# Kernel optimization log

Hardware: AMD Instinct MI355X
Metric: run time of the kernel (lower is better)

## Reference

```python
import jax, jax.numpy as jnp
import numpy as np

TEMPERATURE = 0.07
EPS = 1e-8
LAMBDA_CONTRASTIVE = 0.3
AMBIGUOUS_THRESHOLD = 0.05
LABEL_SMOOTHING = 0.1

B, D, NUM_DIMS, NUM_PIECES = 4096, 256, 19, 1024


def setup_inputs() -> dict:
    key = jax.random.key(0)
    ks = jax.random.split(key, 7)
    return {
        "z_a": jax.random.normal(ks[0], (B, D), dtype=jnp.float32),
        "z_b": jax.random.normal(ks[1], (B, D), dtype=jnp.float32),
        "ranking_logits": jax.random.normal(ks[2], (B, NUM_DIMS), dtype=jnp.float32),
        "labels_a": jax.random.uniform(ks[3], (B, NUM_DIMS), dtype=jnp.float32),
        "labels_b": jax.random.uniform(ks[4], (B, NUM_DIMS), dtype=jnp.float32),
        "piece_ids_a": jax.random.randint(ks[5], (B,), 0, NUM_PIECES, dtype=jnp.int64 if jax.config.jax_enable_x64 else jnp.int32),
        "piece_ids_b": jax.random.randint(ks[6], (B,), 0, NUM_PIECES, dtype=jnp.int64 if jax.config.jax_enable_x64 else jnp.int32),
    }


def _infonce(embeddings, piece_ids, temperature=TEMPERATURE, eps=EPS):
    # embeddings [N, D], piece_ids [N]. Same-piece samples are positives.
    norm = jnp.sqrt(jnp.sum(embeddings * embeddings, axis=-1, keepdims=True))
    z = embeddings / jnp.maximum(norm, eps)  # F.normalize semantics
    sim = (z @ z.T) / temperature  # [N, N]
    n = sim.shape[0]
    eye = jnp.eye(n, dtype=bool)
    piece_mask = piece_ids[None, :] == piece_ids[:, None]
    pos_mask = piece_mask & ~eye
    neg_mask = (~piece_mask) & ~eye
    # row-wise max subtraction (detached in torch) is a no-op on the value since
    # (pos - logsumexp) is shift-invariant; compute stably via masked logsumexp.
    neg_inf = jnp.array(-jnp.inf, sim.dtype)
    neg_lse = jax.scipy.special.logsumexp(jnp.where(neg_mask, sim, neg_inf), axis=-1)  # [N]
    valid_anchor = pos_mask.any(axis=1) & neg_mask.any(axis=1)  # [N]
    pair_mask = pos_mask & valid_anchor[:, None]  # each positive of a valid anchor
    # per-positive term: logsumexp([pos_sim, negs_of_row]) - pos_sim
    lse = jnp.logaddexp(sim, neg_lse[:, None])  # [N, N]
    term = jnp.where(pair_mask, lse - sim, 0.0)
    count = jnp.sum(pair_mask)
    loss = jnp.sum(term) / jnp.maximum(count, 1)
    return jnp.where(count > 0, loss, 0.0)


def _ranking_loss(logits, labels_a, labels_b,
                  ambiguous_threshold=AMBIGUOUS_THRESHOLD,
                  label_smoothing=LABEL_SMOOTHING):
    label_diff = labels_a - labels_b
    targets = (label_diff > 0).astype(logits.dtype)
    non_ambiguous = jnp.abs(label_diff) >= ambiguous_threshold
    targets = targets * (1.0 - label_smoothing) + 0.5 * label_smoothing
    # BCE-with-logits, elementwise, mean over non-ambiguous entries
    bce = jnp.maximum(logits, 0.0) - logits * targets + jnp.log1p(jnp.exp(-jnp.abs(logits)))
    cnt = jnp.sum(non_ambiguous)
    loss = jnp.sum(jnp.where(non_ambiguous, bce, 0.0)) / jnp.maximum(cnt, 1)
    return jnp.where(cnt > 0, loss, 0.0)


def reference(z_a, z_b, ranking_logits, labels_a, labels_b, piece_ids_a, piece_ids_b):
    l_rank = _ranking_loss(ranking_logits, labels_a, labels_b)
    all_z = jnp.concatenate([z_a, z_b], axis=0)        # [2B, D]
    all_pieces = jnp.concatenate([piece_ids_a, piece_ids_b], axis=0)  # [2B]
    l_contrast = _infonce(all_z, all_pieces)
    total = l_rank + LAMBDA_CONTRASTIVE * l_contrast
    return (total, l_rank, l_contrast)
```

## Files before the change

### kernel.cpp

```cpp
#include <hip/hip_runtime.h>
#include <hip/hip_bf16.h>
#include <math.h>

#define NTOT 8192
#define HB   4096
#define DIM  256
#define RANK_N (4096*19)
#define NORM_BLOCKS (NTOT/4)
#define RANK_BLOCKS (RANK_N/256)
#define ZERO_BLOCKS 2
#define INV_T 14.285714285714286f
#define SHIFT 16.0f
#define MAXP  48
#define POST_BLOCKS (NTOT/256)

typedef __attribute__((ext_vector_type(8))) short bf16x8_t;
typedef __attribute__((ext_vector_type(4))) float f32x4_t;

__device__ __forceinline__ unsigned short f2bf(float f) {
  union { float fv; unsigned int u; } v; v.fv = f;
  unsigned int u = v.u;
  unsigned int r = u + 0x7FFFu + ((u >> 16) & 1u);
  return (unsigned short)(r >> 16);
}

__device__ __forceinline__ const float* zrow(const float* za, const float* zb, int g) {
  return g < HB ? za + (size_t)g * DIM : zb + (size_t)(g - HB) * DIM;
}
__device__ __forceinline__ int piece_of(const int* pa, const int* pb, int g) {
  return g < HB ? pa[g] : pb[g - HB];
}

__global__ void k_pre(const float* __restrict__ za, const float* __restrict__ zb,
                      const float* __restrict__ logits, const float* __restrict__ la,
                      const float* __restrict__ lb,
                      const int* __restrict__ pa, const int* __restrict__ pb,
                      unsigned short* __restrict__ zn, float* __restrict__ rank_part,
                      float* __restrict__ neg_s, int* __restrict__ posCount,
                      float* __restrict__ accf, int* __restrict__ done) {
  __shared__ float sred[8];
  int bid = blockIdx.x;
  int t = threadIdx.x;
  if (bid < NORM_BLOCKS) {
    int lane = t & 63, w = t >> 6;
    int row = bid * 4 + w;
    const float* src = zrow(za, zb, row);
    float4 v = *reinterpret_cast<const float4*>(src + lane * 4);
    float ss = v.x * v.x + v.y * v.y + v.z * v.z + v.w * v.w;
    for (int o = 32; o; o >>= 1) ss += __shfl_xor(ss, o, 64);
    float inv = 1.0f / fmaxf(sqrtf(ss), 1e-8f);
    ushort4 o;
    o.x = f2bf(v.x * inv); o.y = f2bf(v.y * inv);
    o.z = f2bf(v.z * inv); o.w = f2bf(v.w * inv);
    *reinterpret_cast<ushort4*>(zn + (size_t)row * DIM + lane * 4) = o;
  } else if (bid < NORM_BLOCKS + RANK_BLOCKS) {
    int rb = bid - NORM_BLOCKS;
    int e = rb * 256 + t;
    float lsum = 0.f, lcnt = 0.f;
    float diff = la[e] - lb[e];
    if (fabsf(diff) >= 0.05f) {
      float x = logits[e];
      float tgt = diff > 0.f ? 0.95f : 0.05f;
      lsum = fmaxf(x, 0.f) - x * tgt + log1pf(__expf(-fabsf(x)));
      lcnt = 1.f;
    }
    for (int o = 32; o; o >>= 1) { lsum += __shfl_xor(lsum, o, 64); lcnt += __shfl_xor(lcnt, o, 64); }
    int w = t >> 6, lane = t & 63;
    if (lane == 0) { sred[w * 2] = lsum; sred[w * 2 + 1] = lcnt; }
    __syncthreads();
    if (t == 0) {
      float S = 0.f, C = 0.f;
      for (int i = 0; i < 4; ++i) { S += sred[i * 2]; C += sred[i * 2 + 1]; }
      rank_part[rb * 2] = S;
      rank_part[rb * 2 + 1] = C;
    }
  } else {
    int z = bid - NORM_BLOCKS - RANK_BLOCKS;
    if (z == 0) {
      for (int k = t; k < NTOT; k += 256) neg_s[k] = 0.f;
      if (t == 0) { accf[0] = 0.f; accf[1] = 0.f; accf[2] = 0.f; accf[3] = 0.f; *done = 0; }
    } else {
      for (int k = t; k < NTOT; k += 256) posCount[k] = 0;
    }
  }
}

__global__ __launch_bounds__(256, 4)
void k_gram(const unsigned short* __restrict__ zn,
            const int* __restrict__ pa, const int* __restrict__ pb,
            float* __restrict__ neg_s, int* __restrict__ posCount,
            float* __restrict__ pos_sims) {
  __shared__ unsigned short Bs[64 * 256];
  __shared__ int Ps[512];
  const int t = threadIdx.x;
  const int lane = t & 63;
  const int w = t >> 6;
  const int l15 = lane & 15;
  const int lg = lane >> 4;
  const int it = blockIdx.x >> 4;
  const int chunk = blockIdx.x & 15;
  const int ibase = it * 128;
  const int jbase0 = chunk * 512;

  Ps[t]       = piece_of(pa, pb, jbase0 + t);
  Ps[t + 256] = piece_of(pa, pb, jbase0 + t + 256);

  bf16x8_t afrag[2][8];
  for (int mt = 0; mt < 2; ++mt) {
    int garow = ibase + w * 32 + mt * 16 + l15;
    const unsigned short* asrc = zn + (size_t)garow * DIM;
    for (int ks = 0; ks < 8; ++ks)
      afrag[mt][ks] = *reinterpret_cast<const bf16x8_t*>(asrc + lg * 8 + ks * 32);
  }

  int prow[8];
  for (int mt = 0; mt < 2; ++mt)
    for (int r = 0; r < 4; ++r)
      prow[mt * 4 + r] = piece_of(pa, pb, ibase + w * 32 + mt * 16 + lg * 4 + r);

  float s[8] = {0.f, 0.f, 0.f, 0.f, 0.f, 0.f, 0.f, 0.f};

  const int tr = t >> 5;
  const int tc = t & 31;
  const unsigned short* gsrc = zn + (size_t)(jbase0 + tr) * DIM + tc * 8;
  unsigned short* lds_dst = &Bs[tr * 256 + ((tc * 8) ^ ((tr & 7) << 3))];

  bf16x8_t pre[8];
#pragma unroll
  for (int i = 0; i < 8; ++i)
    pre[i] = *reinterpret_cast<const bf16x8_t*>(gsrc + (size_t)i * 8 * DIM);

  for (int jt = 0; jt < 8; ++jt) {
    __syncthreads();
#pragma unroll
    for (int i = 0; i < 8; ++i)
      *reinterpret_cast<bf16x8_t*>(lds_dst + i * 8 * 256) = pre[i];
    __syncthreads();
    if (jt < 7) {
      const unsigned short* nsrc = gsrc + (size_t)(jt + 1) * 64 * DIM;
#pragma unroll
      for (int i = 0; i < 8; ++i)
        pre[i] = *reinterpret_cast<const bf16x8_t*>(nsrc + (size_t)i * 8 * DIM);
    }
    for (int ct = 0; ct < 4; ++ct) {
      int jl = jt * 64 + ct * 16 + l15;
      int pc = Ps[jl];
      int jj = jbase0 + jl;
      int brow = ct * 16 + l15;
      f32x4_t acc0 = {0.f, 0.f, 0.f, 0.f};
      f32x4_t acc1 = {0.f, 0.f, 0.f, 0.f};
      for (int ks = 0; ks < 8; ++ks) {
        bf16x8_t bfrag = *reinterpret_cast<const bf16x8_t*>(
            &Bs[brow * 256 + ((lg * 8 + ks * 32) ^ ((brow & 7) << 3))]);
        acc0 = __builtin_amdgcn_mfma_f32_16x16x32_bf16(afrag[0][ks], bfrag, acc0, 0, 0, 0);
        acc1 = __builtin_amdgcn_mfma_f32_16x16x32_bf16(afrag[1][ks], bfrag, acc1, 0, 0, 0);
      }
      for (int r = 0; r < 4; ++r) {
        int gi0 = ibase + w * 32 + lg * 4 + r;
        float sim0 = acc0[r] * INV_T;
        if (pc != prow[r]) {
          s[r] += __expf(sim0 - SHIFT);
        } else if (jj != gi0) {
          int slot = atomicAdd(&posCount[gi0], 1);
          if (slot < MAXP) pos_sims[(size_t)gi0 * MAXP + slot] = sim0;
        }
        int gi1 = gi0 + 16;
        float sim1 = acc1[r] * INV_T;
        if (pc != prow[4 + r]) {
          s[4 + r] += __expf(sim1 - SHIFT);
        } else if (jj != gi1) {
          int slot = atomicAdd(&posCount[gi1], 1);
          if (slot < MAXP) pos_sims[(size_t)gi1 * MAXP + slot] = sim1;
        }
      }
    }
  }
  for (int q = 0; q < 8; ++q) {
    float v = s[q];
    v += __shfl_xor(v, 1, 64);
    v += __shfl_xor(v, 2, 64);
    v += __shfl_xor(v, 4, 64);
    v += __shfl_xor(v, 8, 64);
    if (l15 == 0)
      atomicAdd(&neg_s[ibase + w * 32 + (q >> 2) * 16 + lg * 4 + (q & 3)], v);
  }
}

__global__ void k_post(const float* __restrict__ neg_s,
                       const int* __restrict__ posCount, const float* __restrict__ pos_sims,
                       const float* __restrict__ rank_part,
                       float* __restrict__ accf, int* __restrict__ done,
                       float* __restrict__ out) {
  int t = threadIdx.x;
  int i = blockIdx.x * 256 + t;
  float lsum = 0.f, lcnt = 0.f;
  int posCnt = posCount[i];
  if (posCnt > 0 && posCnt < NTOT - 1) {
    float nlse = SHIFT + logf(neg_s[i]);
    int m = posCnt < MAXP ? posCnt : MAXP;
    for (int s = 0; s < m; ++s) {
      float x = nlse - pos_sims[(size_t)i * MAXP + s];
      lsum += fmaxf(x, 0.f) + log1pf(__expf(-fabsf(x)));
    }
    lcnt = (float)posCnt;
  }
  for (int o = 32; o; o >>= 1) { lsum += __shfl_xor(lsum, o, 64); lcnt += __shfl_xor(lcnt, o, 64); }
  __shared__ float sred[8];
  __shared__ int isLast;
  int w = t >> 6, lane = t & 63;
  if (lane == 0) { sred[w * 2] = lsum; sred[w * 2 + 1] = lcnt; }
  __syncthreads();
  if (t == 0) {
    float S = 0.f, C = 0.f;
    for (int k = 0; k < 4; ++k) { S += sred[k * 2]; C += sred[k * 2 + 1]; }
    atomicAdd(&accf[2], S);
    atomicAdd(&accf[3], C);
    __threadfence();
    int old = atomicAdd(done, 1);
    isLast = (old == POST_BLOCKS - 1);
  }
  __syncthreads();
  if (isLast) {
    __threadfence();
    float rs = 0.f, rc = 0.f;
    for (int rb = t; rb < RANK_BLOCKS; rb += 256) {
      rs += rank_part[rb * 2];
      rc += rank_part[rb * 2 + 1];
    }
    for (int o = 32; o; o >>= 1) { rs += __shfl_xor(rs, o, 64); rc += __shfl_xor(rc, o, 64); }
    if (lane == 0) { sred[w * 2] = rs; sred[w * 2 + 1] = rc; }
    __syncthreads();
    if (t == 0) {
      float RS = 0.f, RC = 0.f;
      for (int k = 0; k < 4; ++k) { RS += sred[k * 2]; RC += sred[k * 2 + 1]; }
      float ps = accf[2], pcn = accf[3];
      float l_rank = RC > 0.f ? RS / RC : 0.f;
      float l_con = pcn > 0.f ? ps / pcn : 0.f;
      out[0] = l_rank + 0.3f * l_con;
      out[1] = l_rank;
      out[2] = l_con;
    }
  }
}

extern "C" void kernel_launch(void* const* d_in, const int* in_sizes, int n_in,
                              void* d_out, int out_size, void* d_ws, size_t ws_size,
                              hipStream_t stream) {
  const float* za     = (const float*)d_in[0];
  const float* zb     = (const float*)d_in[1];
  const float* logits = (const float*)d_in[2];
  const float* la     = (const float*)d_in[3];
  const float* lb     = (const float*)d_in[4];
  const int*   pa     = (const int*)d_in[5];
  const int*   pb     = (const int*)d_in[6];
  float* out = (float*)d_out;

  float* wsf = (float*)d_ws;
  int*   wsi = (int*)d_ws;
  float* accf      = wsf;
  int*   done      = wsi + 4;
  float* rank_part = wsf + 8;
  float* neg_s     = wsf + 616;
  int*   posCount  = wsi + 8808;
  float* pos_sims  = wsf + 17000;
  unsigned short* zn = (unsigned short*)(wsf + 410216);

  k_pre<<<NORM_BLOCKS + RANK_BLOCKS + ZERO_BLOCKS, 256, 0, stream>>>(
      za, zb, logits, la, lb, pa, pb, zn, rank_part, neg_s, posCount, accf, done);
  k_gram<<<1024, 256, 0, stream>>>(zn, pa, pb, neg_s, posCount, pos_sims);
  k_post<<<POST_BLOCKS, 256, 0, stream>>>(neg_s, posCount, pos_sims, rank_part, accf, done, out);
}
```

Before: 177.9 us.

## Load gram B-fragments straight from global memory, dropping LDS staging and barriers

The gram kernel no longer stages 64-row B tiles through shared memory with double-buffered prefetch and block barriers. Each wave now loads its own 16-row B fragments directly from global memory (relying on L2/L1 caching) and reads piece ids directly per column. Loops are fully unrolled and launch bounds are relaxed from 4 to 3 blocks per CU to allow more registers. This removes the barrier and LDS traffic, but each of the four waves in a block now fetches the same B data separately, and global load latency is no longer hidden by an explicit prefetch.

```diff
diff --git a/kernel.cpp b/kernel.cpp
--- a/kernel.cpp
+++ b/kernel.cpp
@@ -85,13 +85,11 @@
   }
 }
 
-__global__ __launch_bounds__(256, 4)
+__global__ __launch_bounds__(256, 3)
 void k_gram(const unsigned short* __restrict__ zn,
             const int* __restrict__ pa, const int* __restrict__ pb,
             float* __restrict__ neg_s, int* __restrict__ posCount,
             float* __restrict__ pos_sims) {
-  __shared__ unsigned short Bs[64 * 256];
-  __shared__ int Ps[512];
   const int t = threadIdx.x;
   const int lane = t & 63;
   const int w = t >> 6;
@@ -102,79 +100,61 @@
   const int ibase = it * 128;
   const int jbase0 = chunk * 512;
 
-  Ps[t]       = piece_of(pa, pb, jbase0 + t);
-  Ps[t + 256] = piece_of(pa, pb, jbase0 + t + 256);
-
   bf16x8_t afrag[2][8];
+#pragma unroll
   for (int mt = 0; mt < 2; ++mt) {
     int garow = ibase + w * 32 + mt * 16 + l15;
     const unsigned short* asrc = zn + (size_t)garow * DIM;
+#pragma unroll
     for (int ks = 0; ks < 8; ++ks)
       afrag[mt][ks] = *reinterpret_cast<const bf16x8_t*>(asrc + lg * 8 + ks * 32);
   }
 
   int prow[8];
+#pragma unroll
   for (int mt = 0; mt < 2; ++mt)
+#pragma unroll
     for (int r = 0; r < 4; ++r)
       prow[mt * 4 + r] = piece_of(pa, pb, ibase + w * 32 + mt * 16 + lg * 4 + r);
 
   float s[8] = {0.f, 0.f, 0.f, 0.f, 0.f, 0.f, 0.f, 0.f};
 
-  const int tr = t >> 5;
-  const int tc = t & 31;
-  const unsigned short* gsrc = zn + (size_t)(jbase0 + tr) * DIM + tc * 8;
-  unsigned short* lds_dst = &Bs[tr * 256 + ((tc * 8) ^ ((tr & 7) << 3))];
-
-  bf16x8_t pre[8];
-#pragma unroll
-  for (int i = 0; i < 8; ++i)
-    pre[i] = *reinterpret_cast<const bf16x8_t*>(gsrc + (size_t)i * 8 * DIM);
-
-  for (int jt = 0; jt < 8; ++jt) {
-    __syncthreads();
-#pragma unroll
-    for (int i = 0; i < 8; ++i)
-      *reinterpret_cast<bf16x8_t*>(lds_dst + i * 8 * 256) = pre[i];
-    __syncthreads();
-    if (jt < 7) {
-      const unsigned short* nsrc = gsrc + (size_t)(jt + 1) * 64 * DIM;
-#pragma unroll
-      for (int i = 0; i < 8; ++i)
-        pre[i] = *reinterpret_cast<const bf16x8_t*>(nsrc + (size_t)i * 8 * DIM);
-    }
-    for (int ct = 0; ct < 4; ++ct) {
-      int jl = jt * 64 + ct * 16 + l15;
-      int pc = Ps[jl];
-      int jj = jbase0 + jl;
-      int brow = ct * 16 + l15;
-      f32x4_t acc0 = {0.f, 0.f, 0.f, 0.f};
-      f32x4_t acc1 = {0.f, 0.f, 0.f, 0.f};
-      for (int ks = 0; ks < 8; ++ks) {
-        bf16x8_t bfrag = *reinterpret_cast<const bf16x8_t*>(
-            &Bs[brow * 256 + ((lg * 8 + ks * 32) ^ ((brow & 7) << 3))]);
-        acc0 = __builtin_amdgcn_mfma_f32_16x16x32_bf16(afrag[0][ks], bfrag, acc0, 0, 0, 0);
-        acc1 = __builtin_amdgcn_mfma_f32_16x16x32_bf16(afrag[1][ks], bfrag, acc1, 0, 0, 0);
+  for (int m = 0; m < 32; ++m) {
+    int jr = jbase0 + m * 16 + l15;
+    int pc = piece_of(pa, pb, jr);
+    const unsigned short* bsrc = zn + (size_t)jr * DIM + lg * 8;
+    bf16x8_t bfrag[8];
+#pragma unroll
+    for (int ks = 0; ks < 8; ++ks)
+      bfrag[ks] = *reinterpret_cast<const bf16x8_t*>(bsrc + ks * 32);
+    f32x4_t acc0 = {0.f, 0.f, 0.f, 0.f};
+    f32x4_t acc1 = {0.f, 0.f, 0.f, 0.f};
+#pragma unroll
+    for (int ks = 0; ks < 8; ++ks) {
+      acc0 = __builtin_amdgcn_mfma_f32_16x16x32_bf16(afrag[0][ks], bfrag[ks], acc0, 0, 0, 0);
+      acc1 = __builtin_amdgcn_mfma_f32_16x16x32_bf16(afrag[1][ks], bfrag[ks], acc1, 0, 0, 0);
+    }
+#pragma unroll
+    for (int r = 0; r < 4; ++r) {
+      int gi0 = ibase + w * 32 + lg * 4 + r;
+      float sim0 = acc0[r] * INV_T;
+      if (pc != prow[r]) {
+        s[r] += __expf(sim0 - SHIFT);
+      } else if (jr != gi0) {
+        int slot = atomicAdd(&posCount[gi0], 1);
+        if (slot < MAXP) pos_sims[(size_t)gi0 * MAXP + slot] = sim0;
       }
-      for (int r = 0; r < 4; ++r) {
-        int gi0 = ibase + w * 32 + lg * 4 + r;
-        float sim0 = acc0[r] * INV_T;
-        if (pc != prow[r]) {
-          s[r] += __expf(sim0 - SHIFT);
-        } else if (jj != gi0) {
-          int slot = atomicAdd(&posCount[gi0], 1);
-          if (slot < MAXP) pos_sims[(size_t)gi0 * MAXP + slot] = sim0;
-        }
-        int gi1 = gi0 + 16;
-        float sim1 = acc1[r] * INV_T;
-        if (pc != prow[4 + r]) {
-          s[4 + r] += __expf(sim1 - SHIFT);
-        } else if (jj != gi1) {
-          int slot = atomicAdd(&posCount[gi1], 1);
-          if (slot < MAXP) pos_sims[(size_t)gi1 * MAXP + slot] = sim1;
-        }
+      int gi1 = gi0 + 16;
+      float sim1 = acc1[r] * INV_T;
+      if (pc != prow[4 + r]) {
+        s[4 + r] += __expf(sim1 - SHIFT);
+      } else if (jr != gi1) {
+        int slot = atomicAdd(&posCount[gi1], 1);
+        if (slot < MAXP) pos_sims[(size_t)gi1 * MAXP + slot] = sim1;
       }
     }
   }
+#pragma unroll
   for (int q = 0; q < 8; ++q) {
     float v = s[q];
     v += __shfl_xor(v, 1, 64);
```

Result: slower. 291.3 us (+63.8%).

## Stage Gram B tiles via direct global-to-LDS loads with double buffering

Applied to the files above, without the earlier changes.

The normalize kernel now writes the bf16 embeddings in a pre-swizzled layout, so the Gram kernel can copy B tiles straight from global memory into LDS with global_load_lds and skip the register round-trip. LDS is double-buffered, so the next tile loads while MFMAs run on the current one, with one barrier per iteration instead of two. Inner loops are fully unrolled. Launch bounds drop from 4 to 2 blocks per CU to make room for the doubled 64 KB LDS footprint, which may cut occupancy and latency hiding.

```diff
diff --git a/kernel.cpp b/kernel.cpp
--- a/kernel.cpp
+++ b/kernel.cpp
@@ -29,6 +29,12 @@
 }
 __device__ __forceinline__ int piece_of(const int* pa, const int* pb, int g) {
   return g < HB ? pa[g] : pb[g - HB];
+}
+
+__device__ __forceinline__ void gload_lds16(const unsigned short* g, unsigned short* l) {
+  __builtin_amdgcn_global_load_lds(
+      (const __attribute__((address_space(1))) unsigned int*)g,
+      (__attribute__((address_space(3))) unsigned int*)l, 16, 0, 0);
 }
 
 __global__ void k_pre(const float* __restrict__ za, const float* __restrict__ zb,
@@ -52,7 +58,8 @@
     ushort4 o;
     o.x = f2bf(v.x * inv); o.y = f2bf(v.y * inv);
     o.z = f2bf(v.z * inv); o.w = f2bf(v.w * inv);
-    *reinterpret_cast<ushort4*>(zn + (size_t)row * DIM + lane * 4) = o;
+    int phys = (((lane >> 1) ^ (row & 7)) << 3) + ((lane & 1) << 2);
+    *reinterpret_cast<ushort4*>(zn + (size_t)row * DIM + phys) = o;
   } else if (bid < NORM_BLOCKS + RANK_BLOCKS) {
     int rb = bid - NORM_BLOCKS;
     int e = rb * 256 + t;
@@ -85,12 +92,12 @@
   }
 }
 
-__global__ __launch_bounds__(256, 4)
+__global__ __launch_bounds__(256, 2)
 void k_gram(const unsigned short* __restrict__ zn,
             const int* __restrict__ pa, const int* __restrict__ pb,
             float* __restrict__ neg_s, int* __restrict__ posCount,
             float* __restrict__ pos_sims) {
-  __shared__ unsigned short Bs[64 * 256];
+  __shared__ unsigned short Bs[2][64 * 256];
   __shared__ int Ps[512];
   const int t = threadIdx.x;
   const int lane = t & 63;
@@ -106,55 +113,62 @@
   Ps[t + 256] = piece_of(pa, pb, jbase0 + t + 256);
 
   bf16x8_t afrag[2][8];
+#pragma unroll
   for (int mt = 0; mt < 2; ++mt) {
     int garow = ibase + w * 32 + mt * 16 + l15;
     const unsigned short* asrc = zn + (size_t)garow * DIM;
+    int sw = garow & 7;
+#pragma unroll
     for (int ks = 0; ks < 8; ++ks)
-      afrag[mt][ks] = *reinterpret_cast<const bf16x8_t*>(asrc + lg * 8 + ks * 32);
+      afrag[mt][ks] = *reinterpret_cast<const bf16x8_t*>(asrc + (((lg + ks * 4) ^ sw) << 3));
   }
 
   int prow[8];
+#pragma unroll
   for (int mt = 0; mt < 2; ++mt)
+#pragma unroll
     for (int r = 0; r < 4; ++r)
       prow[mt * 4 + r] = piece_of(pa, pb, ibase + w * 32 + mt * 16 + lg * 4 + r);
 
   float s[8] = {0.f, 0.f, 0.f, 0.f, 0.f, 0.f, 0.f, 0.f};
 
-  const int tr = t >> 5;
-  const int tc = t & 31;
-  const unsigned short* gsrc = zn + (size_t)(jbase0 + tr) * DIM + tc * 8;
-  unsigned short* lds_dst = &Bs[tr * 256 + ((tc * 8) ^ ((tr & 7) << 3))];
-
-  bf16x8_t pre[8];
-#pragma unroll
-  for (int i = 0; i < 8; ++i)
-    pre[i] = *reinterpret_cast<const bf16x8_t*>(gsrc + (size_t)i * 8 * DIM);
-
+  const int srow = w * 16 + (lane >> 5);
+  const int scol = (lane & 31) * 8;
+
+#define STAGE(buf, jt_)                                                        \
+  {                                                                            \
+    int jb_ = jbase0 + (jt_) * 64;                                             \
+    const unsigned short* g0 = zn + (size_t)(jb_ + srow) * DIM + scol;         \
+    unsigned short* l0 = &Bs[buf][w * 4096];                                   \
+    _Pragma("unroll")                                                          \
+    for (int i_ = 0; i_ < 8; ++i_)                                             \
+      gload_lds16(g0 + (size_t)(2 * i_) * DIM, l0 + i_ * 512);                 \
+  }
+
+  STAGE(0, 0)
+  __syncthreads();
+
+  int cur = 0;
   for (int jt = 0; jt < 8; ++jt) {
-    __syncthreads();
-#pragma unroll
-    for (int i = 0; i < 8; ++i)
-      *reinterpret_cast<bf16x8_t*>(lds_dst + i * 8 * 256) = pre[i];
-    __syncthreads();
-    if (jt < 7) {
-      const unsigned short* nsrc = gsrc + (size_t)(jt + 1) * 64 * DIM;
-#pragma unroll
-      for (int i = 0; i < 8; ++i)
-        pre[i] = *reinterpret_cast<const bf16x8_t*>(nsrc + (size_t)i * 8 * DIM);
-    }
+    if (jt < 7) STAGE(cur ^ 1, jt + 1)
+    const unsigned short* Bb = &Bs[cur][0];
+#pragma unroll
     for (int ct = 0; ct < 4; ++ct) {
       int jl = jt * 64 + ct * 16 + l15;
       int pc = Ps[jl];
       int jj = jbase0 + jl;
       int brow = ct * 16 + l15;
+      int bsw = brow & 7;
+      const unsigned short* bbase = Bb + brow * 256;
       f32x4_t acc0 = {0.f, 0.f, 0.f, 0.f};
       f32x4_t acc1 = {0.f, 0.f, 0.f, 0.f};
+#pragma unroll
       for (int ks = 0; ks < 8; ++ks) {
-        bf16x8_t bfrag = *reinterpret_cast<const bf16x8_t*>(
-            &Bs[brow * 256 + ((lg * 8 + ks * 32) ^ ((brow & 7) << 3))]);
+        bf16x8_t bfrag = *reinterpret_cast<const bf16x8_t*>(bbase + (((lg + ks * 4) ^ bsw) << 3));
         acc0 = __builtin_amdgcn_mfma_f32_16x16x32_bf16(afrag[0][ks], bfrag, acc0, 0, 0, 0);
         acc1 = __builtin_amdgcn_mfma_f32_16x16x32_bf16(afrag[1][ks], bfrag, acc1, 0, 0, 0);
       }
+#pragma unroll
       for (int r = 0; r < 4; ++r) {
         int gi0 = ibase + w * 32 + lg * 4 + r;
         float sim0 = acc0[r] * INV_T;
@@ -174,7 +188,10 @@
         }
       }
     }
-  }
+    __syncthreads();
+    cur ^= 1;
+  }
+#pragma unroll
   for (int q = 0; q < 8; ++q) {
     float v = s[q];
     v += __shfl_xor(v, 1, 64);
@@ -184,6 +201,7 @@
     if (l15 == 0)
       atomicAdd(&neg_s[ibase + w * 32 + (q >> 2) * 16 + lg * 4 + (q & 3)], v);
   }
+#undef STAGE
 }
 
 __global__ void k_post(const float* __restrict__ neg_s,
```

Result: faster. 159.6 us (-10.3%).
